# Optimization experiments

Measured on AMD Instinct MI355X. Metric: run time of the kernel, lower is better.

The kernel has to match this reference:

```python
import jax, jax.numpy as jnp
import numpy as np

N, M_CTX, SIN, YDIM, SPROJ = 16384, 4096, 256, 7, 256


def setup_inputs() -> dict:
    key = jax.random.key(0)
    k1, k2, k3, k4, k5 = jax.random.split(key, 5)
    return {
        "x": jax.random.normal(k1, (N, SIN), dtype=jnp.float32),
        "y": jax.random.normal(k2, (M_CTX, YDIM), dtype=jnp.float32),
        "Wq": jax.random.normal(k3, (SIN, SPROJ), dtype=jnp.float32) / np.sqrt(SIN),
        "Wk": jax.random.normal(k4, (YDIM, SPROJ), dtype=jnp.float32) / np.sqrt(YDIM),
        "Wv": jax.random.normal(k5, (YDIM, SPROJ), dtype=jnp.float32) / np.sqrt(YDIM),
    }


def smooth_softmax(x):
    # softmax over keys (axis=1) blended with 0.1*relu, renormalized
    s = jax.nn.softmax(x, axis=1)
    num = jax.nn.relu(x) * 0.1 + s
    return num / jnp.sum(num, axis=1, keepdims=True)


def reference(x, y, Wq, Wk, Wv):
    XQ = x @ Wq            # [N, P]
    YK = y @ Wk            # [M, P]
    YV = y @ Wv            # [M, P]
    scores = (XQ @ YK.T) / jnp.sqrt(jnp.asarray(YK.shape[1], XQ.dtype))  # [N, M]
    A = smooth_softmax(scores)
    return A @ YV          # [N, P]
```

## Files before the change

### kernel.cpp

```cpp
#include <hip/hip_runtime.h>
#include <hip/hip_bf16.h>

#define N_Q   16384
#define MCTX  4096
#define DSIN  256
#define YDIM  7
#define PDIM  256
#define BK    32

typedef __attribute__((ext_vector_type(8))) short s16x8;
typedef __attribute__((ext_vector_type(4))) float f32x4;
typedef unsigned short u16;

static __device__ __forceinline__ u16 f2bf(float f) {
    union { float f; unsigned u; } v; v.f = f;
    unsigned r = v.u + 0x7fffu + ((v.u >> 16) & 1u);
    return (u16)(r >> 16);
}
static __device__ __forceinline__ float bf2f(u16 h) {
    union { unsigned u; float f; } v; v.u = ((unsigned)h) << 16;
    return v.f;
}
static __device__ __forceinline__ f32x4 mfma16(s16x8 a, s16x8 b, f32x4 c) {
    return __builtin_amdgcn_mfma_f32_16x16x32_bf16(a, b, c, 0, 0, 0);
}
static __device__ __forceinline__ void gload_lds16(const u16* g, u16* l) {
    __builtin_amdgcn_global_load_lds(
        (const __attribute__((address_space(1))) unsigned int*)(g),
        (__attribute__((address_space(3))) unsigned int*)(l), 16, 0, 0);
}

__global__ void k_prep(const float* __restrict__ Wq, u16* __restrict__ WtH,
                       u16* __restrict__ WtL, const float* __restrict__ y,
                       const float* __restrict__ Wk, const float* __restrict__ Wv,
                       u16* __restrict__ YK, u16* __restrict__ YVb) {
    if (blockIdx.x < PDIM) {
        int n = blockIdx.x;
        int k = threadIdx.x;
        float w = Wq[(size_t)k * PDIM + n];
        u16 h = f2bf(w);
        WtH[(size_t)n * DSIN + k] = h;
        WtL[(size_t)n * DSIN + k] = f2bf(w - bf2f(h));
    } else {
        int kb = blockIdx.x - PDIM;
        int p  = threadIdx.x;
        float wk[YDIM], wv[YDIM];
#pragma unroll
        for (int j = 0; j < YDIM; ++j) {
            wk[j] = Wk[(size_t)j * PDIM + p];
            wv[j] = Wv[(size_t)j * PDIM + p];
        }
        u16 vbuf[32];
#pragma unroll
        for (int m = 0; m < 32; ++m) {
            int key = kb * 32 + m;
            float ak = 0.f, av = 0.f;
#pragma unroll
            for (int j = 0; j < YDIM; ++j) {
                float yy = y[(size_t)key * YDIM + j];
                ak += yy * wk[j];
                av += yy * wv[j];
            }
            YK[(size_t)key * PDIM + p] = f2bf(ak * 0.0625f);
            vbuf[m] = f2bf(av);
        }
        s16x8* dst = (s16x8*)(YVb + ((size_t)kb * PDIM + p) * 32);
#pragma unroll
        for (int c = 0; c < 4; ++c) dst[c] = ((s16x8*)vbuf)[c];
    }
}

__global__ __launch_bounds__(256, 2) void k_xq(const float* __restrict__ x,
                                               const u16* __restrict__ WtH,
                                               const u16* __restrict__ WtL,
                                               u16* __restrict__ XQ) {
    __shared__ u16 xH[32 * 256];
    __shared__ u16 xL[32 * 256];
    const int tid = threadIdx.x;
    const int rowg0 = blockIdx.x * 32;
#pragma unroll
    for (int i = 0; i < 4; ++i) {
        int row = (tid >> 5) + i * 8;
        int c32 = tid & 31;
        const float* px = x + (size_t)(rowg0 + row) * DSIN + c32 * 8;
        float4 a = *(const float4*)px;
        float4 b = *(const float4*)(px + 4);
        float vals[8] = {a.x, a.y, a.z, a.w, b.x, b.y, b.z, b.w};
        s16x8 h, l;
#pragma unroll
        for (int j = 0; j < 8; ++j) {
            u16 hh = f2bf(vals[j]);
            h[j] = (short)hh;
            l[j] = (short)f2bf(vals[j] - bf2f(hh));
        }
        int pc = c32 ^ (row & 7);
        *(s16x8*)(xH + row * 256 + pc * 8) = h;
        *(s16x8*)(xL + row * 256 + pc * 8) = l;
    }
    __syncthreads();

    const int wave = tid >> 6, lane = tid & 63;
    const int quad = lane >> 4, m16 = lane & 15;
    const int rh = wave & 1, ph = wave >> 1;
    const int rowl = rh * 16 + m16;
    const int swz = rowl & 7;
    s16x8 ah[8], al[8];
#pragma unroll
    for (int kf = 0; kf < 8; ++kf) {
        int pc = (kf * 4 + quad) ^ swz;
        ah[kf] = *(const s16x8*)(xH + rowl * 256 + pc * 8);
        al[kf] = *(const s16x8*)(xL + rowl * 256 + pc * 8);
    }
#pragma unroll
    for (int ptl = 0; ptl < 8; ++ptl) {
        int pt = ph * 8 + ptl;
        f32x4 acc = (f32x4){0.f, 0.f, 0.f, 0.f};
#pragma unroll
        for (int kf = 0; kf < 8; ++kf) {
            size_t idx = (size_t)(pt * 16 + m16) * DSIN + kf * 32 + quad * 8;
            s16x8 bh = *(const s16x8*)(WtH + idx);
            s16x8 bl = *(const s16x8*)(WtL + idx);
            acc = mfma16(ah[kf], bh, acc);
            acc = mfma16(al[kf], bh, acc);
            acc = mfma16(ah[kf], bl, acc);
        }
#pragma unroll
        for (int r = 0; r < 4; ++r)
            XQ[(size_t)(rowg0 + rh * 16 + quad * 4 + r) * PDIM + pt * 16 + m16] =
                f2bf(acc[r]);
    }
}

__global__ __launch_bounds__(256, 2) void k_attn(const u16* __restrict__ XQ,
                                                 const u16* __restrict__ YK,
                                                 const u16* __restrict__ YVb,
                                                 u16* __restrict__ accE,
                                                 u16* __restrict__ accR,
                                                 float* __restrict__ lsum,
                                                 float* __restrict__ rsum,
                                                 int msPerSplit) {
    __shared__ u16 Kt[32 * 256];
    __shared__ u16 Pe[64 * 40];
    __shared__ u16 Pr[64 * 40];

    const int tid = threadIdx.x;
    const int wave = tid >> 6, lane = tid & 63;
    const int quad = lane >> 4, m16 = lane & 15;
    const int split = blockIdx.y;
    const int qbase = blockIdx.x * 64;
    const int key_begin = split * msPerSplit;
    const int iters = msPerSplit / BK;
    const int pslice = wave * 64;
    const int swz = m16 & 7;

    s16x8 qf[8];
    const u16* qp = XQ + (size_t)(qbase + wave * 16 + m16) * DSIN;
#pragma unroll
    for (int kf = 0; kf < 8; ++kf)
        qf[kf] = *(const s16x8*)(qp + kf * 32 + quad * 8);

    f32x4 aE[4][4], aR[4][4];
#pragma unroll
    for (int g = 0; g < 4; ++g)
#pragma unroll
        for (int t = 0; t < 4; ++t) {
            aE[g][t] = (f32x4){0.f, 0.f, 0.f, 0.f};
            aR[g][t] = (f32x4){0.f, 0.f, 0.f, 0.f};
        }
    float lacc[4] = {0.f, 0.f, 0.f, 0.f}, racc[4] = {0.f, 0.f, 0.f, 0.f};

    auto stage = [&](int key0) {
#pragma unroll
        for (int c = 0; c < 4; ++c) {
            int l = (wave * 4 + c) * 64 + lane;
            int r = l >> 5;
            int sc = (l & 31) ^ (r & 7);
            gload_lds16(YK + (size_t)(key0 + r) * DSIN + sc * 8,
                        Kt + (size_t)(wave * 4 + c) * 512);
        }
    };
    stage(key_begin);

    for (int it = 0; it < iters; ++it) {
        const int key0 = key_begin + it * BK;
        __syncthreads();

        f32x4 s0 = (f32x4){0.f, 0.f, 0.f, 0.f};
        f32x4 s1 = (f32x4){0.f, 0.f, 0.f, 0.f};
        __builtin_amdgcn_s_setprio(1);
#pragma unroll
        for (int kf = 0; kf < 8; ++kf) {
            int pc = (kf * 4 + quad) ^ swz;
            s16x8 b0 = *(const s16x8*)(Kt + m16 * 256 + pc * 8);
            s16x8 b1 = *(const s16x8*)(Kt + (16 + m16) * 256 + pc * 8);
            s0 = mfma16(qf[kf], b0, s0);
            s1 = mfma16(qf[kf], b1, s1);
        }
        __builtin_amdgcn_s_setprio(0);
#pragma unroll
        for (int r = 0; r < 4; ++r) {
            float e0 = __expf(s0[r]), e1 = __expf(s1[r]);
            float rl0 = fmaxf(s0[r], 0.f), rl1 = fmaxf(s1[r], 0.f);
            lacc[r] += e0 + e1;
            racc[r] += rl0 + rl1;
            int row = wave * 16 + quad * 4 + r;
            Pe[row * 40 + m16]      = f2bf(e0);
            Pe[row * 40 + 16 + m16] = f2bf(e1);
            Pr[row * 40 + m16]      = f2bf(rl0);
            Pr[row * 40 + 16 + m16] = f2bf(rl1);
        }
        __syncthreads();

        s16x8 vf[4];
        const u16* vb = YVb + (size_t)((key0 >> 5) * PDIM) * 32;
#pragma unroll
        for (int t = 0; t < 4; ++t)
            vf[t] = *(const s16x8*)(vb + (size_t)(pslice + t * 16 + m16) * 32 + quad * 8);

        if (it + 1 < iters) stage(key0 + BK);

        __builtin_amdgcn_s_setprio(1);
#pragma unroll
        for (int g = 0; g < 4; ++g) {
            s16x8 pa = *(const s16x8*)(Pe + (g * 16 + m16) * 40 + quad * 8);
            s16x8 pb = *(const s16x8*)(Pr + (g * 16 + m16) * 40 + quad * 8);
#pragma unroll
            for (int t = 0; t < 4; ++t) {
                aE[g][t] = mfma16(pa, vf[t], aE[g][t]);
                aR[g][t] = mfma16(pb, vf[t], aR[g][t]);
            }
        }
        __builtin_amdgcn_s_setprio(0);
    }

    size_t ob = ((size_t)split * N_Q + qbase) * PDIM;
#pragma unroll
    for (int g = 0; g < 4; ++g)
#pragma unroll
        for (int t = 0; t < 4; ++t)
#pragma unroll
            for (int r = 0; r < 4; ++r) {
                size_t o = ob + (size_t)(g * 16 + quad * 4 + r) * PDIM + pslice + t * 16 + m16;
                accE[o] = f2bf(aE[g][t][r]);
                accR[o] = f2bf(aR[g][t][r]);
            }
#pragma unroll
    for (int r = 0; r < 4; ++r) {
        lacc[r] += __shfl_xor(lacc[r], 1);
        lacc[r] += __shfl_xor(lacc[r], 2);
        lacc[r] += __shfl_xor(lacc[r], 4);
        lacc[r] += __shfl_xor(lacc[r], 8);
        racc[r] += __shfl_xor(racc[r], 1);
        racc[r] += __shfl_xor(racc[r], 2);
        racc[r] += __shfl_xor(racc[r], 4);
        racc[r] += __shfl_xor(racc[r], 8);
    }
    if (m16 < 4) {
        float lv = (m16 == 0) ? lacc[0] : (m16 == 1) ? lacc[1] : (m16 == 2) ? lacc[2] : lacc[3];
        float rv = (m16 == 0) ? racc[0] : (m16 == 1) ? racc[1] : (m16 == 2) ? racc[2] : racc[3];
        int row = split * N_Q + qbase + wave * 16 + quad * 4 + m16;
        lsum[row] = lv;
        rsum[row] = rv;
    }
}

__global__ void k_comb(const u16* __restrict__ accE, const u16* __restrict__ accR,
                       const float* __restrict__ lsum, const float* __restrict__ rsum,
                       float* __restrict__ out, int nsplit) {
    int row = blockIdx.x * 8 + (threadIdx.x >> 5);
    int col = (threadIdx.x & 31) * 8;
    size_t idx = (size_t)row * PDIM + col;
    const size_t NP = (size_t)N_Q * PDIM;
    float E[8] = {0.f, 0.f, 0.f, 0.f, 0.f, 0.f, 0.f, 0.f};
    float R[8] = {0.f, 0.f, 0.f, 0.f, 0.f, 0.f, 0.f, 0.f};
    float L = 0.f, Rs = 0.f;
    for (int s = 0; s < nsplit; ++s) {
        s16x8 e = *(const s16x8*)(accE + s * NP + idx);
        s16x8 r = *(const s16x8*)(accR + s * NP + idx);
#pragma unroll
        for (int j = 0; j < 8; ++j) {
            E[j] += bf2f((u16)e[j]);
            R[j] += bf2f((u16)r[j]);
        }
        L  += lsum[(size_t)s * N_Q + row];
        Rs += rsum[(size_t)s * N_Q + row];
    }
    float invL = 1.f / L, invD = 1.f / (1.f + 0.1f * Rs);
    float4 o0, o1;
    o0.x = (0.1f * R[0] + E[0] * invL) * invD;
    o0.y = (0.1f * R[1] + E[1] * invL) * invD;
    o0.z = (0.1f * R[2] + E[2] * invL) * invD;
    o0.w = (0.1f * R[3] + E[3] * invL) * invD;
    o1.x = (0.1f * R[4] + E[4] * invL) * invD;
    o1.y = (0.1f * R[5] + E[5] * invL) * invD;
    o1.z = (0.1f * R[6] + E[6] * invL) * invD;
    o1.w = (0.1f * R[7] + E[7] * invL) * invD;
    *(float4*)(out + idx) = o0;
    *(float4*)(out + idx + 4) = o1;
}

extern "C" void kernel_launch(void* const* d_in, const int* in_sizes, int n_in,
                              void* d_out, int out_size, void* d_ws, size_t ws_size,
                              hipStream_t stream) {
    const float* x  = (const float*)d_in[0];
    const float* y  = (const float*)d_in[1];
    const float* Wq = (const float*)d_in[2];
    const float* Wk = (const float*)d_in[3];
    const float* Wv = (const float*)d_in[4];
    float* out = (float*)d_out;

    char* ws = (char*)d_ws;
    size_t off = 0;
    auto take = [&](size_t bytes) -> char* {
        char* p = ws + off;
        off += (bytes + 255) & ~(size_t)255;
        return p;
    };
    u16* XQ  = (u16*)take((size_t)N_Q * PDIM * 2);
    u16* WtH = (u16*)take((size_t)PDIM * DSIN * 2);
    u16* WtL = (u16*)take((size_t)PDIM * DSIN * 2);
    u16* YK  = (u16*)take((size_t)MCTX * PDIM * 2);
    u16* YVb = (u16*)take((size_t)MCTX * PDIM * 2);

    size_t perSplit = (size_t)N_Q * PDIM * 2 * 2 + (size_t)N_Q * 4 * 2 + 1024;
    int nsplit = (ws_size >= off + 2 * perSplit + 4096) ? 2 : 1;

    u16*   accE = (u16*)take((size_t)nsplit * N_Q * PDIM * 2);
    u16*   accR = (u16*)take((size_t)nsplit * N_Q * PDIM * 2);
    float* lsum = (float*)take((size_t)nsplit * N_Q * 4);
    float* rsum = (float*)take((size_t)nsplit * N_Q * 4);

    hipLaunchKernelGGL(k_prep, dim3(PDIM + MCTX/32), dim3(256), 0, stream,
                       Wq, WtH, WtL, y, Wk, Wv, YK, YVb);
    hipLaunchKernelGGL(k_xq,   dim3(N_Q/32), dim3(256), 0, stream, x, WtH, WtL, XQ);
    hipLaunchKernelGGL(k_attn, dim3(N_Q/64, nsplit), dim3(256), 0, stream,
                       XQ, YK, YVb, accE, accR, lsum, rsum, MCTX / nsplit);
    hipLaunchKernelGGL(k_comb, dim3(N_Q/8), dim3(256), 0, stream,
                       accE, accR, lsum, rsum, out, nsplit);
}
```

Before: 228.1 us.

## Pre-pack YK into MFMA fragment layout and load keys directly from global

The prep kernel now writes the scaled key projection in a layout where each wave's MFMA B-fragment is a contiguous 1 KB block indexed by lane. The attention kernel drops the LDS staging of key tiles (global_load_lds with swizzle) and reads the fragments straight from global or L2 into registers. This removes LDS traffic and LDS footprint for K, which may raise occupancy. In exchange, key loads are no longer prefetched a tile ahead, so their latency sits in front of the score MFMAs, and every wave fetches the full key tile itself.

```diff
diff --git a/kernel.cpp b/kernel.cpp
--- a/kernel.cpp
+++ b/kernel.cpp
@@ -24,16 +24,11 @@
 static __device__ __forceinline__ f32x4 mfma16(s16x8 a, s16x8 b, f32x4 c) {
     return __builtin_amdgcn_mfma_f32_16x16x32_bf16(a, b, c, 0, 0, 0);
 }
-static __device__ __forceinline__ void gload_lds16(const u16* g, u16* l) {
-    __builtin_amdgcn_global_load_lds(
-        (const __attribute__((address_space(1))) unsigned int*)(g),
-        (__attribute__((address_space(3))) unsigned int*)(l), 16, 0, 0);
-}
 
 __global__ void k_prep(const float* __restrict__ Wq, u16* __restrict__ WtH,
                        u16* __restrict__ WtL, const float* __restrict__ y,
                        const float* __restrict__ Wk, const float* __restrict__ Wv,
-                       u16* __restrict__ YK, u16* __restrict__ YVb) {
+                       u16* __restrict__ YKb, u16* __restrict__ YVb) {
     if (blockIdx.x < PDIM) {
         int n = blockIdx.x;
         int k = threadIdx.x;
@@ -50,7 +45,7 @@
             wk[j] = Wk[(size_t)j * PDIM + p];
             wv[j] = Wv[(size_t)j * PDIM + p];
         }
-        u16 vbuf[32];
+        u16 vbuf[32], akb[32];
 #pragma unroll
         for (int m = 0; m < 32; ++m) {
             int key = kb * 32 + m;
@@ -61,12 +56,22 @@
                 ak += yy * wk[j];
                 av += yy * wv[j];
             }
-            YK[(size_t)key * PDIM + p] = f2bf(ak * 0.0625f);
+            akb[m] = f2bf(ak * 0.0625f);
             vbuf[m] = f2bf(av);
         }
         s16x8* dst = (s16x8*)(YVb + ((size_t)kb * PDIM + p) * 32);
 #pragma unroll
         for (int c = 0; c < 4; ++c) dst[c] = ((s16x8*)vbuf)[c];
+        int kf = p >> 5;
+        int qp = (p >> 3) & 3;
+        int jj = p & 7;
+        size_t base = ((size_t)kb * 8 + kf) * 1024;
+#pragma unroll
+        for (int m = 0; m < 32; ++m) {
+            int kh = m >> 4;
+            int l  = qp * 16 + (m & 15);
+            YKb[base + (size_t)kh * 512 + l * 8 + jj] = akb[m];
+        }
     }
 }
 
@@ -132,14 +137,13 @@
 }
 
 __global__ __launch_bounds__(256, 2) void k_attn(const u16* __restrict__ XQ,
-                                                 const u16* __restrict__ YK,
+                                                 const u16* __restrict__ YKb,
                                                  const u16* __restrict__ YVb,
                                                  u16* __restrict__ accE,
                                                  u16* __restrict__ accR,
                                                  float* __restrict__ lsum,
                                                  float* __restrict__ rsum,
                                                  int msPerSplit) {
-    __shared__ u16 Kt[32 * 256];
     __shared__ u16 Pe[64 * 40];
     __shared__ u16 Pr[64 * 40];
 
@@ -151,7 +155,6 @@
     const int key_begin = split * msPerSplit;
     const int iters = msPerSplit / BK;
     const int pslice = wave * 64;
-    const int swz = m16 & 7;
 
     s16x8 qf[8];
     const u16* qp = XQ + (size_t)(qbase + wave * 16 + m16) * DSIN;
@@ -169,30 +172,18 @@
         }
     float lacc[4] = {0.f, 0.f, 0.f, 0.f}, racc[4] = {0.f, 0.f, 0.f, 0.f};
 
-    auto stage = [&](int key0) {
-#pragma unroll
-        for (int c = 0; c < 4; ++c) {
-            int l = (wave * 4 + c) * 64 + lane;
-            int r = l >> 5;
-            int sc = (l & 31) ^ (r & 7);
-            gload_lds16(YK + (size_t)(key0 + r) * DSIN + sc * 8,
-                        Kt + (size_t)(wave * 4 + c) * 512);
-        }
-    };
-    stage(key_begin);
-
     for (int it = 0; it < iters; ++it) {
         const int key0 = key_begin + it * BK;
         __syncthreads();
 
+        const u16* kbase = YKb + (size_t)(key0 >> 5) * 8192;
         f32x4 s0 = (f32x4){0.f, 0.f, 0.f, 0.f};
         f32x4 s1 = (f32x4){0.f, 0.f, 0.f, 0.f};
         __builtin_amdgcn_s_setprio(1);
 #pragma unroll
         for (int kf = 0; kf < 8; ++kf) {
-            int pc = (kf * 4 + quad) ^ swz;
-            s16x8 b0 = *(const s16x8*)(Kt + m16 * 256 + pc * 8);
-            s16x8 b1 = *(const s16x8*)(Kt + (16 + m16) * 256 + pc * 8);
+            s16x8 b0 = *(const s16x8*)(kbase + (size_t)(kf * 2 + 0) * 512 + lane * 8);
+            s16x8 b1 = *(const s16x8*)(kbase + (size_t)(kf * 2 + 1) * 512 + lane * 8);
             s0 = mfma16(qf[kf], b0, s0);
             s1 = mfma16(qf[kf], b1, s1);
         }
@@ -216,8 +207,6 @@
 #pragma unroll
         for (int t = 0; t < 4; ++t)
             vf[t] = *(const s16x8*)(vb + (size_t)(pslice + t * 16 + m16) * 32 + quad * 8);
-
-        if (it + 1 < iters) stage(key0 + BK);
 
         __builtin_amdgcn_s_setprio(1);
 #pragma unroll
@@ -319,7 +308,7 @@
     u16* XQ  = (u16*)take((size_t)N_Q * PDIM * 2);
     u16* WtH = (u16*)take((size_t)PDIM * DSIN * 2);
     u16* WtL = (u16*)take((size_t)PDIM * DSIN * 2);
-    u16* YK  = (u16*)take((size_t)MCTX * PDIM * 2);
+    u16* YKb = (u16*)take((size_t)MCTX * PDIM * 2);
     u16* YVb = (u16*)take((size_t)MCTX * PDIM * 2);
 
     size_t perSplit = (size_t)N_Q * PDIM * 2 * 2 + (size_t)N_Q * 4 * 2 + 1024;
@@ -331,10 +320,10 @@
     float* rsum = (float*)take((size_t)nsplit * N_Q * 4);
 
     hipLaunchKernelGGL(k_prep, dim3(PDIM + MCTX/32), dim3(256), 0, stream,
-                       Wq, WtH, WtL, y, Wk, Wv, YK, YVb);
+                       Wq, WtH, WtL, y, Wk, Wv, YKb, YVb);
     hipLaunchKernelGGL(k_xq,   dim3(N_Q/32), dim3(256), 0, stream, x, WtH, WtL, XQ);
     hipLaunchKernelGGL(k_attn, dim3(N_Q/64, nsplit), dim3(256), 0, stream,
-                       XQ, YK, YVb, accE, accR, lsum, rsum, MCTX / nsplit);
+                       XQ, YKb, YVb, accE, accR, lsum, rsum, MCTX / nsplit);
     hipLaunchKernelGGL(k_comb, dim3(N_Q/8), dim3(256), 0, stream,
                        accE, accR, lsum, rsum, out, nsplit);
 }
```

After: 303.8 us. 33.2% more time.

## Keep probability tiles in registers by transposing score MFMA and permuting key rows

Applied to the files above, without the earlier changes.

The score MFMA operands are swapped so each lane holds score values in the layout the PV MFMA needs as its A operand. Key rows are permuted during staging so the register fragments line up. This removes the Pe/Pr LDS round trip and its bank traffic. Each wave now computes all 256 output columns for its own 16 query rows instead of a 64-column slice for all 64 rows, so V fragments are loaded from global in chunks interleaved with the MFMAs, which increases per-wave V traffic.

```diff
diff --git a/kernel.cpp b/kernel.cpp
--- a/kernel.cpp
+++ b/kernel.cpp
@@ -140,8 +140,6 @@
                                                  float* __restrict__ rsum,
                                                  int msPerSplit) {
     __shared__ u16 Kt[32 * 256];
-    __shared__ u16 Pe[64 * 40];
-    __shared__ u16 Pr[64 * 40];
 
     const int tid = threadIdx.x;
     const int wave = tid >> 6, lane = tid & 63;
@@ -150,7 +148,6 @@
     const int qbase = blockIdx.x * 64;
     const int key_begin = split * msPerSplit;
     const int iters = msPerSplit / BK;
-    const int pslice = wave * 64;
     const int swz = m16 & 7;
 
     s16x8 qf[8];
@@ -159,23 +156,22 @@
     for (int kf = 0; kf < 8; ++kf)
         qf[kf] = *(const s16x8*)(qp + kf * 32 + quad * 8);
 
-    f32x4 aE[4][4], aR[4][4];
-#pragma unroll
-    for (int g = 0; g < 4; ++g)
-#pragma unroll
-        for (int t = 0; t < 4; ++t) {
-            aE[g][t] = (f32x4){0.f, 0.f, 0.f, 0.f};
-            aR[g][t] = (f32x4){0.f, 0.f, 0.f, 0.f};
-        }
-    float lacc[4] = {0.f, 0.f, 0.f, 0.f}, racc[4] = {0.f, 0.f, 0.f, 0.f};
+    f32x4 aE[16], aR[16];
+#pragma unroll
+    for (int t = 0; t < 16; ++t) {
+        aE[t] = (f32x4){0.f, 0.f, 0.f, 0.f};
+        aR[t] = (f32x4){0.f, 0.f, 0.f, 0.f};
+    }
+    float lacc = 0.f, racc = 0.f;
 
     auto stage = [&](int key0) {
 #pragma unroll
         for (int c = 0; c < 4; ++c) {
             int l = (wave * 4 + c) * 64 + lane;
             int r = l >> 5;
+            int sg = ((r >> 2) & 3) * 8 + (r & 3) + ((r >> 4) << 2);
             int sc = (l & 31) ^ (r & 7);
-            gload_lds16(YK + (size_t)(key0 + r) * DSIN + sc * 8,
+            gload_lds16(YK + (size_t)(key0 + sg) * DSIN + sc * 8,
                         Kt + (size_t)(wave * 4 + c) * 512);
         }
     };
@@ -191,76 +187,91 @@
 #pragma unroll
         for (int kf = 0; kf < 8; ++kf) {
             int pc = (kf * 4 + quad) ^ swz;
-            s16x8 b0 = *(const s16x8*)(Kt + m16 * 256 + pc * 8);
-            s16x8 b1 = *(const s16x8*)(Kt + (16 + m16) * 256 + pc * 8);
-            s0 = mfma16(qf[kf], b0, s0);
-            s1 = mfma16(qf[kf], b1, s1);
+            s16x8 a0 = *(const s16x8*)(Kt + m16 * 256 + pc * 8);
+            s16x8 a1 = *(const s16x8*)(Kt + (16 + m16) * 256 + pc * 8);
+            s0 = mfma16(a0, qf[kf], s0);
+            s1 = mfma16(a1, qf[kf], s1);
         }
         __builtin_amdgcn_s_setprio(0);
+
+        float e0[4], e1[4], r0[4], r1[4];
 #pragma unroll
         for (int r = 0; r < 4; ++r) {
-            float e0 = __expf(s0[r]), e1 = __expf(s1[r]);
-            float rl0 = fmaxf(s0[r], 0.f), rl1 = fmaxf(s1[r], 0.f);
-            lacc[r] += e0 + e1;
-            racc[r] += rl0 + rl1;
-            int row = wave * 16 + quad * 4 + r;
-            Pe[row * 40 + m16]      = f2bf(e0);
-            Pe[row * 40 + 16 + m16] = f2bf(e1);
-            Pr[row * 40 + m16]      = f2bf(rl0);
-            Pr[row * 40 + 16 + m16] = f2bf(rl1);
-        }
+            e0[r] = __expf(s0[r]);  r0[r] = fmaxf(s0[r], 0.f);
+            e1[r] = __expf(s1[r]);  r1[r] = fmaxf(s1[r], 0.f);
+            lacc += e0[r] + e1[r];
+            racc += r0[r] + r1[r];
+        }
+        union { unsigned u[4]; s16x8 v; } pa, pb;
+        pa.u[0] = ((unsigned)f2bf(e0[1]) << 16) | f2bf(e0[0]);
+        pa.u[1] = ((unsigned)f2bf(e0[3]) << 16) | f2bf(e0[2]);
+        pa.u[2] = ((unsigned)f2bf(e1[1]) << 16) | f2bf(e1[0]);
+        pa.u[3] = ((unsigned)f2bf(e1[3]) << 16) | f2bf(e1[2]);
+        pb.u[0] = ((unsigned)f2bf(r0[1]) << 16) | f2bf(r0[0]);
+        pb.u[1] = ((unsigned)f2bf(r0[3]) << 16) | f2bf(r0[2]);
+        pb.u[2] = ((unsigned)f2bf(r1[1]) << 16) | f2bf(r1[0]);
+        pb.u[3] = ((unsigned)f2bf(r1[3]) << 16) | f2bf(r1[2]);
+
         __syncthreads();
 
-        s16x8 vf[4];
         const u16* vb = YVb + (size_t)((key0 >> 5) * PDIM) * 32;
-#pragma unroll
-        for (int t = 0; t < 4; ++t)
-            vf[t] = *(const s16x8*)(vb + (size_t)(pslice + t * 16 + m16) * 32 + quad * 8);
+        s16x8 vfa[4], vfb[4];
+#pragma unroll
+        for (int i = 0; i < 4; ++i)
+            vfa[i] = *(const s16x8*)(vb + (size_t)(i * 16 + m16) * 32 + quad * 8);
+#pragma unroll
+        for (int i = 0; i < 4; ++i)
+            vfb[i] = *(const s16x8*)(vb + (size_t)((4 + i) * 16 + m16) * 32 + quad * 8);
 
         if (it + 1 < iters) stage(key0 + BK);
 
         __builtin_amdgcn_s_setprio(1);
 #pragma unroll
-        for (int g = 0; g < 4; ++g) {
-            s16x8 pa = *(const s16x8*)(Pe + (g * 16 + m16) * 40 + quad * 8);
-            s16x8 pb = *(const s16x8*)(Pr + (g * 16 + m16) * 40 + quad * 8);
-#pragma unroll
-            for (int t = 0; t < 4; ++t) {
-                aE[g][t] = mfma16(pa, vf[t], aE[g][t]);
-                aR[g][t] = mfma16(pb, vf[t], aR[g][t]);
-            }
+        for (int t = 0; t < 4; ++t) {
+            aE[t] = mfma16(pa.v, vfa[t], aE[t]);
+            aR[t] = mfma16(pb.v, vfa[t], aR[t]);
+        }
+#pragma unroll
+        for (int i = 0; i < 4; ++i)
+            vfa[i] = *(const s16x8*)(vb + (size_t)((8 + i) * 16 + m16) * 32 + quad * 8);
+#pragma unroll
+        for (int t = 0; t < 4; ++t) {
+            aE[4 + t] = mfma16(pa.v, vfb[t], aE[4 + t]);
+            aR[4 + t] = mfma16(pb.v, vfb[t], aR[4 + t]);
+        }
+#pragma unroll
+        for (int i = 0; i < 4; ++i)
+            vfb[i] = *(const s16x8*)(vb + (size_t)((12 + i) * 16 + m16) * 32 + quad * 8);
+#pragma unroll
+        for (int t = 0; t < 4; ++t) {
+            aE[8 + t] = mfma16(pa.v, vfa[t], aE[8 + t]);
+            aR[8 + t] = mfma16(pb.v, vfa[t], aR[8 + t]);
+        }
+#pragma unroll
+        for (int t = 0; t < 4; ++t) {
+            aE[12 + t] = mfma16(pa.v, vfb[t], aE[12 + t]);
+            aR[12 + t] = mfma16(pb.v, vfb[t], aR[12 + t]);
         }
         __builtin_amdgcn_s_setprio(0);
     }
 
     size_t ob = ((size_t)split * N_Q + qbase) * PDIM;
 #pragma unroll
-    for (int g = 0; g < 4; ++g)
-#pragma unroll
-        for (int t = 0; t < 4; ++t)
-#pragma unroll
-            for (int r = 0; r < 4; ++r) {
-                size_t o = ob + (size_t)(g * 16 + quad * 4 + r) * PDIM + pslice + t * 16 + m16;
-                accE[o] = f2bf(aE[g][t][r]);
-                accR[o] = f2bf(aR[g][t][r]);
-            }
-#pragma unroll
-    for (int r = 0; r < 4; ++r) {
-        lacc[r] += __shfl_xor(lacc[r], 1);
-        lacc[r] += __shfl_xor(lacc[r], 2);
-        lacc[r] += __shfl_xor(lacc[r], 4);
-        lacc[r] += __shfl_xor(lacc[r], 8);
-        racc[r] += __shfl_xor(racc[r], 1);
-        racc[r] += __shfl_xor(racc[r], 2);
-        racc[r] += __shfl_xor(racc[r], 4);
-        racc[r] += __shfl_xor(racc[r], 8);
-    }
-    if (m16 < 4) {
-        float lv = (m16 == 0) ? lacc[0] : (m16 == 1) ? lacc[1] : (m16 == 2) ? lacc[2] : lacc[3];
-        float rv = (m16 == 0) ? racc[0] : (m16 == 1) ? racc[1] : (m16 == 2) ? racc[2] : racc[3];
-        int row = split * N_Q + qbase + wave * 16 + quad * 4 + m16;
-        lsum[row] = lv;
-        rsum[row] = rv;
+    for (int t = 0; t < 16; ++t)
+#pragma unroll
+        for (int r = 0; r < 4; ++r) {
+            size_t o = ob + (size_t)(wave * 16 + quad * 4 + r) * PDIM + t * 16 + m16;
+            accE[o] = f2bf(aE[t][r]);
+            accR[o] = f2bf(aR[t][r]);
+        }
+    lacc += __shfl_xor(lacc, 16);
+    lacc += __shfl_xor(lacc, 32);
+    racc += __shfl_xor(racc, 16);
+    racc += __shfl_xor(racc, 32);
+    if (lane < 16) {
+        int row = split * N_Q + qbase + wave * 16 + m16;
+        lsum[row] = lacc;
+        rsum[row] = racc;
     }
 }
 
```

New measurement: 297.5 us. 1.3x slower.

## Switch attention kernel to 32x32x16 MFMA with LDS-staged Q and repacked V

Applied to the files above, without the earlier changes.

Rewrites the attention kernel to use 32x32x16 bf16 MFMA tiles instead of 16x16x32. Q is staged into shared memory, and YV is repacked in the prep kernel into a layout that matches the 32x32 operand fragments. Only two of the four waves now compute scores and exponentials, while all four waves do the PV accumulation over 32-query by 128-column tiles. The larger tiles cut per-FLOP LDS operand traffic. In exchange, half the waves sit idle during the QK phase, and the 32 KB Q buffer raises LDS use, which may limit occupancy.

```diff
diff --git a/kernel.cpp b/kernel.cpp
--- a/kernel.cpp
+++ b/kernel.cpp
@@ -10,6 +10,7 @@
 
 typedef __attribute__((ext_vector_type(8))) short s16x8;
 typedef __attribute__((ext_vector_type(4))) float f32x4;
+typedef __attribute__((ext_vector_type(16))) float f32x16;
 typedef unsigned short u16;
 
 static __device__ __forceinline__ u16 f2bf(float f) {
@@ -24,6 +25,9 @@
 static __device__ __forceinline__ f32x4 mfma16(s16x8 a, s16x8 b, f32x4 c) {
     return __builtin_amdgcn_mfma_f32_16x16x32_bf16(a, b, c, 0, 0, 0);
 }
+static __device__ __forceinline__ f32x16 mfma32(s16x8 a, s16x8 b, f32x16 c) {
+    return __builtin_amdgcn_mfma_f32_32x32x16_bf16(a, b, c, 0, 0, 0);
+}
 static __device__ __forceinline__ void gload_lds16(const u16* g, u16* l) {
     __builtin_amdgcn_global_load_lds(
         (const __attribute__((address_space(1))) unsigned int*)(g),
@@ -33,7 +37,7 @@
 __global__ void k_prep(const float* __restrict__ Wq, u16* __restrict__ WtH,
                        u16* __restrict__ WtL, const float* __restrict__ y,
                        const float* __restrict__ Wk, const float* __restrict__ Wv,
-                       u16* __restrict__ YK, u16* __restrict__ YVb) {
+                       u16* __restrict__ YK, u16* __restrict__ YVb32) {
     if (blockIdx.x < PDIM) {
         int n = blockIdx.x;
         int k = threadIdx.x;
@@ -64,9 +68,12 @@
             YK[(size_t)key * PDIM + p] = f2bf(ak * 0.0625f);
             vbuf[m] = f2bf(av);
         }
-        s16x8* dst = (s16x8*)(YVb + ((size_t)kb * PDIM + p) * 32);
-#pragma unroll
-        for (int c = 0; c < 4; ++c) dst[c] = ((s16x8*)vbuf)[c];
+#pragma unroll
+        for (int m = 0; m < 32; ++m) {
+            int c = m >> 4, hh = (m >> 3) & 1, j = m & 7;
+            size_t idx = ((((size_t)kb * 2 + c) * 8 + (p >> 5)) * 64 + hh * 32 + (p & 31)) * 8 + j;
+            YVb32[idx] = vbuf[m];
+        }
     }
 }
 
@@ -133,134 +140,140 @@
 
 __global__ __launch_bounds__(256, 2) void k_attn(const u16* __restrict__ XQ,
                                                  const u16* __restrict__ YK,
-                                                 const u16* __restrict__ YVb,
+                                                 const u16* __restrict__ YVb32,
                                                  u16* __restrict__ accE,
                                                  u16* __restrict__ accR,
                                                  float* __restrict__ lsum,
                                                  float* __restrict__ rsum,
                                                  int msPerSplit) {
+    __shared__ u16 Qt[64 * 256];
     __shared__ u16 Kt[32 * 256];
     __shared__ u16 Pe[64 * 40];
     __shared__ u16 Pr[64 * 40];
 
     const int tid = threadIdx.x;
     const int wave = tid >> 6, lane = tid & 63;
-    const int quad = lane >> 4, m16 = lane & 15;
+    const int l31 = lane & 31, h = lane >> 5;
     const int split = blockIdx.y;
     const int qbase = blockIdx.x * 64;
     const int key_begin = split * msPerSplit;
     const int iters = msPerSplit / BK;
-    const int pslice = wave * 64;
-    const int swz = m16 & 7;
-
-    s16x8 qf[8];
-    const u16* qp = XQ + (size_t)(qbase + wave * 16 + m16) * DSIN;
-#pragma unroll
-    for (int kf = 0; kf < 8; ++kf)
-        qf[kf] = *(const s16x8*)(qp + kf * 32 + quad * 8);
-
-    f32x4 aE[4][4], aR[4][4];
-#pragma unroll
-    for (int g = 0; g < 4; ++g)
-#pragma unroll
-        for (int t = 0; t < 4; ++t) {
-            aE[g][t] = (f32x4){0.f, 0.f, 0.f, 0.f};
-            aR[g][t] = (f32x4){0.f, 0.f, 0.f, 0.f};
-        }
-    float lacc[4] = {0.f, 0.f, 0.f, 0.f}, racc[4] = {0.f, 0.f, 0.f, 0.f};
-
+    const int qh = wave >> 1, ph = wave & 1;
+    const int swq = l31 & 7;
+
+    for (int rnd = 0; rnd < 8; ++rnd) {
+        int L = rnd * 256 + tid;
+        int r = L >> 5;
+        int lc = (L & 31) ^ (r & 7);
+        gload_lds16(XQ + (size_t)(qbase + r) * 256 + lc * 8, Qt + (size_t)L * 8);
+    }
     auto stage = [&](int key0) {
 #pragma unroll
         for (int c = 0; c < 4; ++c) {
-            int l = (wave * 4 + c) * 64 + lane;
-            int r = l >> 5;
-            int sc = (l & 31) ^ (r & 7);
-            gload_lds16(YK + (size_t)(key0 + r) * DSIN + sc * 8,
-                        Kt + (size_t)(wave * 4 + c) * 512);
+            int L = (wave * 4 + c) * 64 + lane;
+            int r = L >> 5;
+            int kap = ((r >> 4) << 4) | (((r >> 2) & 1) << 3) | (((r >> 3) & 1) << 2) | (r & 3);
+            int lc = (L & 31) ^ (r & 7);
+            gload_lds16(YK + (size_t)(key0 + kap) * 256 + lc * 8, Kt + (size_t)L * 8);
         }
     };
     stage(key_begin);
+
+    f32x16 aE[4], aR[4];
+#pragma unroll
+    for (int t = 0; t < 4; ++t)
+#pragma unroll
+        for (int r = 0; r < 16; ++r) { aE[t][r] = 0.f; aR[t][r] = 0.f; }
+    float lacc = 0.f, racc = 0.f;
 
     for (int it = 0; it < iters; ++it) {
         const int key0 = key_begin + it * BK;
         __syncthreads();
 
-        f32x4 s0 = (f32x4){0.f, 0.f, 0.f, 0.f};
-        f32x4 s1 = (f32x4){0.f, 0.f, 0.f, 0.f};
-        __builtin_amdgcn_s_setprio(1);
-#pragma unroll
-        for (int kf = 0; kf < 8; ++kf) {
-            int pc = (kf * 4 + quad) ^ swz;
-            s16x8 b0 = *(const s16x8*)(Kt + m16 * 256 + pc * 8);
-            s16x8 b1 = *(const s16x8*)(Kt + (16 + m16) * 256 + pc * 8);
-            s0 = mfma16(qf[kf], b0, s0);
-            s1 = mfma16(qf[kf], b1, s1);
-        }
-        __builtin_amdgcn_s_setprio(0);
-#pragma unroll
-        for (int r = 0; r < 4; ++r) {
-            float e0 = __expf(s0[r]), e1 = __expf(s1[r]);
-            float rl0 = fmaxf(s0[r], 0.f), rl1 = fmaxf(s1[r], 0.f);
-            lacc[r] += e0 + e1;
-            racc[r] += rl0 + rl1;
-            int row = wave * 16 + quad * 4 + r;
-            Pe[row * 40 + m16]      = f2bf(e0);
-            Pe[row * 40 + 16 + m16] = f2bf(e1);
-            Pr[row * 40 + m16]      = f2bf(rl0);
-            Pr[row * 40 + 16 + m16] = f2bf(rl1);
+        s16x8 vf[4][2];
+#pragma unroll
+        for (int pt = 0; pt < 4; ++pt)
+#pragma unroll
+            for (int c = 0; c < 2; ++c)
+                vf[pt][c] = *(const s16x8*)(YVb32 +
+                    ((((size_t)(key0 >> 5) * 2 + c) * 8 + (ph * 4 + pt)) * 64 + lane) * 8);
+
+        if (wave < 2) {
+            f32x16 s;
+#pragma unroll
+            for (int r = 0; r < 16; ++r) s[r] = 0.f;
+            __builtin_amdgcn_s_setprio(1);
+#pragma unroll
+            for (int kf = 0; kf < 16; ++kf) {
+                int pc = (kf * 2 + h) ^ swq;
+                s16x8 a = *(const s16x8*)(Kt + (size_t)l31 * 256 + pc * 8);
+                s16x8 b = *(const s16x8*)(Qt + (size_t)(wave * 32 + l31) * 256 + pc * 8);
+                s = mfma32(a, b, s);
+            }
+            __builtin_amdgcn_s_setprio(0);
+            float e[16], rl[16];
+#pragma unroll
+            for (int r = 0; r < 16; ++r) {
+                e[r] = __expf(s[r]);
+                rl[r] = fmaxf(s[r], 0.f);
+                lacc += e[r];
+                racc += rl[r];
+            }
+            int q = wave * 32 + l31;
+#pragma unroll
+            for (int c = 0; c < 2; ++c) {
+                union { unsigned u[4]; s16x8 v; } pe_, pr_;
+#pragma unroll
+                for (int wi = 0; wi < 4; ++wi) {
+                    pe_.u[wi] = ((unsigned)f2bf(e[c * 8 + 2 * wi + 1]) << 16) | f2bf(e[c * 8 + 2 * wi]);
+                    pr_.u[wi] = ((unsigned)f2bf(rl[c * 8 + 2 * wi + 1]) << 16) | f2bf(rl[c * 8 + 2 * wi]);
+                }
+                int pc = (c * 2 + h) ^ (q & 3);
+                *(s16x8*)(Pe + q * 40 + pc * 8) = pe_.v;
+                *(s16x8*)(Pr + q * 40 + pc * 8) = pr_.v;
+            }
         }
         __syncthreads();
 
-        s16x8 vf[4];
-        const u16* vb = YVb + (size_t)((key0 >> 5) * PDIM) * 32;
-#pragma unroll
-        for (int t = 0; t < 4; ++t)
-            vf[t] = *(const s16x8*)(vb + (size_t)(pslice + t * 16 + m16) * 32 + quad * 8);
-
         if (it + 1 < iters) stage(key0 + BK);
 
-        __builtin_amdgcn_s_setprio(1);
-#pragma unroll
-        for (int g = 0; g < 4; ++g) {
-            s16x8 pa = *(const s16x8*)(Pe + (g * 16 + m16) * 40 + quad * 8);
-            s16x8 pb = *(const s16x8*)(Pr + (g * 16 + m16) * 40 + quad * 8);
-#pragma unroll
-            for (int t = 0; t < 4; ++t) {
-                aE[g][t] = mfma16(pa, vf[t], aE[g][t]);
-                aR[g][t] = mfma16(pb, vf[t], aR[g][t]);
-            }
-        }
-        __builtin_amdgcn_s_setprio(0);
+        {
+            int q = qh * 32 + l31;
+            int sw = q & 3;
+            s16x8 pe0 = *(const s16x8*)(Pe + q * 40 + ((0 + h) ^ sw) * 8);
+            s16x8 pe1 = *(const s16x8*)(Pe + q * 40 + ((2 + h) ^ sw) * 8);
+            s16x8 pr0 = *(const s16x8*)(Pr + q * 40 + ((0 + h) ^ sw) * 8);
+            s16x8 pr1 = *(const s16x8*)(Pr + q * 40 + ((2 + h) ^ sw) * 8);
+            __builtin_amdgcn_s_setprio(1);
+#pragma unroll
+            for (int pt = 0; pt < 4; ++pt) {
+                aE[pt] = mfma32(pe0, vf[pt][0], aE[pt]);
+                aE[pt] = mfma32(pe1, vf[pt][1], aE[pt]);
+                aR[pt] = mfma32(pr0, vf[pt][0], aR[pt]);
+                aR[pt] = mfma32(pr1, vf[pt][1], aR[pt]);
+            }
+            __builtin_amdgcn_s_setprio(0);
+        }
     }
 
     size_t ob = ((size_t)split * N_Q + qbase) * PDIM;
 #pragma unroll
-    for (int g = 0; g < 4; ++g)
-#pragma unroll
-        for (int t = 0; t < 4; ++t)
-#pragma unroll
-            for (int r = 0; r < 4; ++r) {
-                size_t o = ob + (size_t)(g * 16 + quad * 4 + r) * PDIM + pslice + t * 16 + m16;
-                accE[o] = f2bf(aE[g][t][r]);
-                accR[o] = f2bf(aR[g][t][r]);
-            }
-#pragma unroll
-    for (int r = 0; r < 4; ++r) {
-        lacc[r] += __shfl_xor(lacc[r], 1);
-        lacc[r] += __shfl_xor(lacc[r], 2);
-        lacc[r] += __shfl_xor(lacc[r], 4);
-        lacc[r] += __shfl_xor(lacc[r], 8);
-        racc[r] += __shfl_xor(racc[r], 1);
-        racc[r] += __shfl_xor(racc[r], 2);
-        racc[r] += __shfl_xor(racc[r], 4);
-        racc[r] += __shfl_xor(racc[r], 8);
-    }
-    if (m16 < 4) {
-        float lv = (m16 == 0) ? lacc[0] : (m16 == 1) ? lacc[1] : (m16 == 2) ? lacc[2] : lacc[3];
-        float rv = (m16 == 0) ? racc[0] : (m16 == 1) ? racc[1] : (m16 == 2) ? racc[2] : racc[3];
-        int row = split * N_Q + qbase + wave * 16 + quad * 4 + m16;
-        lsum[row] = lv;
-        rsum[row] = rv;
+    for (int pt = 0; pt < 4; ++pt)
+#pragma unroll
+        for (int r = 0; r < 16; ++r) {
+            int qrow = qh * 32 + (r & 3) + 8 * (r >> 2) + 4 * h;
+            int p = ph * 128 + pt * 32 + l31;
+            accE[ob + (size_t)qrow * PDIM + p] = f2bf(aE[pt][r]);
+            accR[ob + (size_t)qrow * PDIM + p] = f2bf(aR[pt][r]);
+        }
+    if (wave < 2) {
+        lacc += __shfl_xor(lacc, 32);
+        racc += __shfl_xor(racc, 32);
+        if (lane < 32) {
+            int row = split * N_Q + qbase + wave * 32 + lane;
+            lsum[row] = lacc;
+            rsum[row] = racc;
+        }
     }
 }
 
@@ -316,11 +329,11 @@
         off += (bytes + 255) & ~(size_t)255;
         return p;
     };
-    u16* XQ  = (u16*)take((size_t)N_Q * PDIM * 2);
-    u16* WtH = (u16*)take((size_t)PDIM * DSIN * 2);
-    u16* WtL = (u16*)take((size_t)PDIM * DSIN * 2);
-    u16* YK  = (u16*)take((size_t)MCTX * PDIM * 2);
-    u16* YVb = (u16*)take((size_t)MCTX * PDIM * 2);
+    u16* XQ    = (u16*)take((size_t)N_Q * PDIM * 2);
+    u16* WtH   = (u16*)take((size_t)PDIM * DSIN * 2);
+    u16* WtL   = (u16*)take((size_t)PDIM * DSIN * 2);
+    u16* YK    = (u16*)take((size_t)MCTX * PDIM * 2);
+    u16* YVb32 = (u16*)take((size_t)MCTX * PDIM * 2);
 
     size_t perSplit = (size_t)N_Q * PDIM * 2 * 2 + (size_t)N_Q * 4 * 2 + 1024;
     int nsplit = (ws_size >= off + 2 * perSplit + 4096) ? 2 : 1;
@@ -331,10 +344,10 @@
     float* rsum = (float*)take((size_t)nsplit * N_Q * 4);
 
     hipLaunchKernelGGL(k_prep, dim3(PDIM + MCTX/32), dim3(256), 0, stream,
-                       Wq, WtH, WtL, y, Wk, Wv, YK, YVb);
+                       Wq, WtH, WtL, y, Wk, Wv, YK, YVb32);
     hipLaunchKernelGGL(k_xq,   dim3(N_Q/32), dim3(256), 0, stream, x, WtH, WtL, XQ);
     hipLaunchKernelGGL(k_attn, dim3(N_Q/64, nsplit), dim3(256), 0, stream,
-                       XQ, YK, YVb, accE, accR, lsum, rsum, MCTX / nsplit);
+                       XQ, YK, YVb32, accE, accR, lsum, rsum, MCTX / nsplit);
     hipLaunchKernelGGL(k_comb, dim3(N_Q/8), dim3(256), 0, stream,
                        accE, accR, lsum, rsum, out, nsplit);
 }
```

Measured after the change: 321.9 us. +41.1%, slower.
